# Kernel tuning notes

Measured on AMD Instinct MI355X. Metric: run time of the kernel, lower is better.

Reference implementation:

```python
import jax, jax.numpy as jnp
import numpy as np

EPS = 1e-8  # torch F.cosine_similarity eps


def setup_inputs() -> dict:
    key = jax.random.key(0)
    k1, _ = jax.random.split(key)
    h = jax.random.normal(k1, (8, 2048, 128), dtype=jnp.float32)  # [B, N, D]
    temperature = jnp.array(1.0, dtype=jnp.float32)  # learnable scalar param
    return {"h": h, "temperature": temperature}


def reference(h, temperature):
    # Cosine similarity = (h_i . h_j) / (max(||h_i||, eps) * max(||h_j||, eps)).
    # Normalize rows first, then a single GEMM -> avoids the O(N^2*D) broadcast
    # intermediate the torch code materializes.
    norm = jnp.maximum(jnp.linalg.norm(h, axis=-1, keepdims=True), EPS)  # [B, N, 1]
    hn = h / norm                                                        # [B, N, D]
    sim = jnp.einsum("bnd,bmd->bnm", hn, hn)                             # [B, N, N]
    adj = jax.nn.softmax(sim / temperature, axis=-1)
    return adj
```

## Files before the change

### kernel.cpp

```cpp
#include <hip/hip_runtime.h>
#include <hip/hip_bf16.h>
#include <stdint.h>

#define NB 8
#define NN 2048
#define ND 128

typedef __attribute__((ext_vector_type(8))) short short8;
typedef __attribute__((ext_vector_type(4))) float f32x4;

__device__ __forceinline__ uint32_t pack_bf16(float a, float b) {
    unsigned short ua = __builtin_bit_cast(unsigned short, __float2bfloat16(a));
    unsigned short ub = __builtin_bit_cast(unsigned short, __float2bfloat16(b));
    return (uint32_t)ua | ((uint32_t)ub << 16);
}
__device__ __forceinline__ float unpk_lo(uint32_t p) { return __builtin_bit_cast(float, p << 16); }
__device__ __forceinline__ float unpk_hi(uint32_t p) { return __builtin_bit_cast(float, p & 0xffff0000u); }

__global__ __launch_bounds__(256) void adjnorm_kernel(const float* __restrict__ h,
                                                      unsigned short* __restrict__ hn) {
    const int row  = blockIdx.x * 4 + (threadIdx.x >> 6);
    const int lane = threadIdx.x & 63;
    const float2 v = reinterpret_cast<const float2*>(h + (size_t)row * ND)[lane];
    float ss = v.x * v.x + v.y * v.y;
    #pragma unroll
    for (int m = 32; m >= 1; m >>= 1) ss += __shfl_xor(ss, m);
    const float nrm = fmaxf(sqrtf(ss), 1e-8f);
    const float inv = 1.0f / nrm;
    reinterpret_cast<uint32_t*>(hn + (size_t)row * ND)[lane] = pack_bf16(v.x * inv, v.y * inv);
}

__global__ __launch_bounds__(512) void adjmain_kernel(const unsigned short* __restrict__ hn,
                                                      const float* __restrict__ tptr,
                                                      float* __restrict__ out) {
    const int b       = blockIdx.y;
    const int rowBase = blockIdx.x * 32;
    const int lane = threadIdx.x & 63;
    const int wid  = threadIdx.x >> 6;
    const int cq   = wid & 3;
    const int rh   = wid >> 2;
    const int l15  = lane & 15;
    const int g    = lane >> 4;

    const float invt = 1.0f / tptr[0];

    const unsigned short* Hb = hn + (size_t)b * NN * ND;

    short8 afrag[4];
    {
        const unsigned short* ap = Hb + (size_t)(rowBase + rh * 16 + l15) * ND + g * 8;
        #pragma unroll
        for (int c = 0; c < 4; ++c)
            afrag[c] = *reinterpret_cast<const short8*>(ap + c * 32);
    }

    const int colBase = cq * 512;
    float rs[4] = {0.f, 0.f, 0.f, 0.f};
    uint32_t pp[32][2];

    #pragma unroll
    for (int t = 0; t < 32; ++t) {
        const unsigned short* bp = Hb + (size_t)(colBase + t * 16 + l15) * ND + g * 8;
        f32x4 acc = {0.f, 0.f, 0.f, 0.f};
        #pragma unroll
        for (int c = 0; c < 4; ++c) {
            const short8 bfrag = *reinterpret_cast<const short8*>(bp + c * 32);
            acc = __builtin_amdgcn_mfma_f32_16x16x32_bf16(afrag[c], bfrag, acc, 0, 0, 0);
        }
        const float p0 = __expf((acc[0] - 1.0f) * invt);
        const float p1 = __expf((acc[1] - 1.0f) * invt);
        const float p2 = __expf((acc[2] - 1.0f) * invt);
        const float p3 = __expf((acc[3] - 1.0f) * invt);
        rs[0] += p0; rs[1] += p1; rs[2] += p2; rs[3] += p3;
        pp[t][0] = pack_bf16(p0, p1);
        pp[t][1] = pack_bf16(p2, p3);
    }

    #pragma unroll
    for (int r = 0; r < 4; ++r) {
        #pragma unroll
        for (int m = 1; m < 16; m <<= 1) rs[r] += __shfl_xor(rs[r], m);
    }

    __shared__ float rsum_lds[2][4][16];
    if (l15 == 0) {
        #pragma unroll
        for (int r = 0; r < 4; ++r) rsum_lds[rh][cq][g * 4 + r] = rs[r];
    }
    __syncthreads();
    float invs[4];
    #pragma unroll
    for (int r = 0; r < 4; ++r) {
        const int rr = g * 4 + r;
        const float s = rsum_lds[rh][0][rr] + rsum_lds[rh][1][rr] +
                        rsum_lds[rh][2][rr] + rsum_lds[rh][3][rr];
        invs[r] = 1.0f / s;
    }

    float* orow = out + ((size_t)b * NN + rowBase + rh * 16 + g * 4) * NN + colBase + l15;
    #pragma unroll
    for (int t = 0; t < 32; ++t) {
        const int co = t * 16;
        orow[(size_t)0 * NN + co] = unpk_lo(pp[t][0]) * invs[0];
        orow[(size_t)1 * NN + co] = unpk_hi(pp[t][0]) * invs[1];
        orow[(size_t)2 * NN + co] = unpk_lo(pp[t][1]) * invs[2];
        orow[(size_t)3 * NN + co] = unpk_hi(pp[t][1]) * invs[3];
    }
}

extern "C" void kernel_launch(void* const* d_in, const int* in_sizes, int n_in,
                              void* d_out, int out_size, void* d_ws, size_t ws_size,
                              hipStream_t stream) {
    const float* h  = (const float*)d_in[0];
    const float* tp = (const float*)d_in[1];
    unsigned short* hn = (unsigned short*)d_ws;
    float* out = (float*)d_out;

    hipLaunchKernelGGL(adjnorm_kernel, dim3(NB * NN / 4), dim3(256), 0, stream, h, hn);
    hipLaunchKernelGGL(adjmain_kernel, dim3(NN / 32, NB), dim3(512), 0, stream, hn, tp, out);
}
```

Baseline: 203.0 us.

## Use 16-row blocks with 8 column-split waves and double-buffer B loads

```diff
diff --git a/kernel.cpp b/kernel.cpp
--- a/kernel.cpp
+++ b/kernel.cpp
@@ -34,11 +34,9 @@
                                                       const float* __restrict__ tptr,
                                                       float* __restrict__ out) {
     const int b       = blockIdx.y;
-    const int rowBase = blockIdx.x * 32;
+    const int rowBase = blockIdx.x * 16;
     const int lane = threadIdx.x & 63;
-    const int wid  = threadIdx.x >> 6;
-    const int cq   = wid & 3;
-    const int rh   = wid >> 2;
+    const int w    = threadIdx.x >> 6;
     const int l15  = lane & 15;
     const int g    = lane >> 4;
 
@@ -48,33 +46,51 @@
 
     short8 afrag[4];
     {
-        const unsigned short* ap = Hb + (size_t)(rowBase + rh * 16 + l15) * ND + g * 8;
+        const unsigned short* ap = Hb + (size_t)(rowBase + l15) * ND + g * 8;
         #pragma unroll
         for (int c = 0; c < 4; ++c)
             afrag[c] = *reinterpret_cast<const short8*>(ap + c * 32);
     }
 
-    const int colBase = cq * 512;
+    const unsigned short* colPtr = Hb + (size_t)(w * 256 + l15) * ND + g * 8;
+
     float rs[4] = {0.f, 0.f, 0.f, 0.f};
-    uint32_t pp[32][2];
+    uint32_t pp[16][2];
+    short8 bA[4], bB[4];
 
+#define LOADB(dst, T) do {                                                      \
+        const unsigned short* _bp = colPtr + (size_t)(T) * 16 * ND;             \
+        dst[0] = *reinterpret_cast<const short8*>(_bp);                         \
+        dst[1] = *reinterpret_cast<const short8*>(_bp + 32);                    \
+        dst[2] = *reinterpret_cast<const short8*>(_bp + 64);                    \
+        dst[3] = *reinterpret_cast<const short8*>(_bp + 96);                    \
+    } while (0)
+
+#define COMPUTE(T, BUF) do {                                                    \
+        f32x4 acc = {0.f, 0.f, 0.f, 0.f};                                       \
+        acc = __builtin_amdgcn_mfma_f32_16x16x32_bf16(afrag[0], BUF[0], acc, 0, 0, 0); \
+        acc = __builtin_amdgcn_mfma_f32_16x16x32_bf16(afrag[1], BUF[1], acc, 0, 0, 0); \
+        acc = __builtin_amdgcn_mfma_f32_16x16x32_bf16(afrag[2], BUF[2], acc, 0, 0, 0); \
+        acc = __builtin_amdgcn_mfma_f32_16x16x32_bf16(afrag[3], BUF[3], acc, 0, 0, 0); \
+        const float p0 = __expf((acc[0] - 1.0f) * invt);                        \
+        const float p1 = __expf((acc[1] - 1.0f) * invt);                        \
+        const float p2 = __expf((acc[2] - 1.0f) * invt);                        \
+        const float p3 = __expf((acc[3] - 1.0f) * invt);                        \
+        rs[0] += p0; rs[1] += p1; rs[2] += p2; rs[3] += p3;                     \
+        pp[T][0] = pack_bf16(p0, p1);                                           \
+        pp[T][1] = pack_bf16(p2, p3);                                           \
+    } while (0)
+
+    LOADB(bA, 0);
     #pragma unroll
-    for (int t = 0; t < 32; ++t) {
-        const unsigned short* bp = Hb + (size_t)(colBase + t * 16 + l15) * ND + g * 8;
-        f32x4 acc = {0.f, 0.f, 0.f, 0.f};
-        #pragma unroll
-        for (int c = 0; c < 4; ++c) {
-            const short8 bfrag = *reinterpret_cast<const short8*>(bp + c * 32);
-            acc = __builtin_amdgcn_mfma_f32_16x16x32_bf16(afrag[c], bfrag, acc, 0, 0, 0);
-        }
-        const float p0 = __expf((acc[0] - 1.0f) * invt);
-        const float p1 = __expf((acc[1] - 1.0f) * invt);
-        const float p2 = __expf((acc[2] - 1.0f) * invt);
-        const float p3 = __expf((acc[3] - 1.0f) * invt);
-        rs[0] += p0; rs[1] += p1; rs[2] += p2; rs[3] += p3;
-        pp[t][0] = pack_bf16(p0, p1);
-        pp[t][1] = pack_bf16(p2, p3);
+    for (int tt = 0; tt < 8; ++tt) {
+        LOADB(bB, 2 * tt + 1);
+        COMPUTE(2 * tt, bA);
+        if (tt < 7) LOADB(bA, 2 * tt + 2);
+        COMPUTE(2 * tt + 1, bB);
     }
+#undef LOADB
+#undef COMPUTE
 
     #pragma unroll
     for (int r = 0; r < 4; ++r) {
@@ -82,24 +98,25 @@
         for (int m = 1; m < 16; m <<= 1) rs[r] += __shfl_xor(rs[r], m);
     }
 
-    __shared__ float rsum_lds[2][4][16];
+    __shared__ float rsum_lds[8][16];
     if (l15 == 0) {
         #pragma unroll
-        for (int r = 0; r < 4; ++r) rsum_lds[rh][cq][g * 4 + r] = rs[r];
+        for (int r = 0; r < 4; ++r) rsum_lds[w][g * 4 + r] = rs[r];
     }
     __syncthreads();
     float invs[4];
     #pragma unroll
     for (int r = 0; r < 4; ++r) {
         const int rr = g * 4 + r;
-        const float s = rsum_lds[rh][0][rr] + rsum_lds[rh][1][rr] +
-                        rsum_lds[rh][2][rr] + rsum_lds[rh][3][rr];
+        float s = 0.f;
+        #pragma unroll
+        for (int ww = 0; ww < 8; ++ww) s += rsum_lds[ww][rr];
         invs[r] = 1.0f / s;
     }
 
-    float* orow = out + ((size_t)b * NN + rowBase + rh * 16 + g * 4) * NN + colBase + l15;
+    float* orow = out + ((size_t)b * NN + rowBase + g * 4) * NN + w * 256 + l15;
     #pragma unroll
-    for (int t = 0; t < 32; ++t) {
+    for (int t = 0; t < 16; ++t) {
         const int co = t * 16;
         orow[(size_t)0 * NN + co] = unpk_lo(pp[t][0]) * invs[0];
         orow[(size_t)1 * NN + co] = unpk_hi(pp[t][0]) * invs[1];
@@ -117,5 +134,5 @@
     float* out = (float*)d_out;
 
     hipLaunchKernelGGL(adjnorm_kernel, dim3(NB * NN / 4), dim3(256), 0, stream, h, hn);
-    hipLaunchKernelGGL(adjmain_kernel, dim3(NN / 32, NB), dim3(512), 0, stream, hn, tp, out);
+    hipLaunchKernelGGL(adjmain_kernel, dim3(NN / 16, NB), dim3(512), 0, stream, hn, tp, out);
 }
```

Measured after the change: 197.9 us. 2.5% less time.

## Stage B tiles in LDS via async global_load_lds and transpose MFMA for vector stores

Applied to the files above, without the earlier changes.

```diff
diff --git a/kernel.cpp b/kernel.cpp
--- a/kernel.cpp
+++ b/kernel.cpp
@@ -5,6 +5,7 @@
 #define NB 8
 #define NN 2048
 #define ND 128
+#define NT 32
 
 typedef __attribute__((ext_vector_type(8))) short short8;
 typedef __attribute__((ext_vector_type(4))) float f32x4;
@@ -16,6 +17,12 @@
 }
 __device__ __forceinline__ float unpk_lo(uint32_t p) { return __builtin_bit_cast(float, p << 16); }
 __device__ __forceinline__ float unpk_hi(uint32_t p) { return __builtin_bit_cast(float, p & 0xffff0000u); }
+
+__device__ __forceinline__ void gload_lds16(const void* g, void* l) {
+    __builtin_amdgcn_global_load_lds(
+        (const __attribute__((address_space(1))) unsigned int*)g,
+        (__attribute__((address_space(3))) unsigned int*)l, 16, 0, 0);
+}
 
 __global__ __launch_bounds__(256) void adjnorm_kernel(const float* __restrict__ h,
                                                       unsigned short* __restrict__ hn) {
@@ -30,9 +37,9 @@
     reinterpret_cast<uint32_t*>(hn + (size_t)row * ND)[lane] = pack_bf16(v.x * inv, v.y * inv);
 }
 
-__global__ __launch_bounds__(512) void adjmain_kernel(const unsigned short* __restrict__ hn,
-                                                      const float* __restrict__ tptr,
-                                                      float* __restrict__ out) {
+__global__ __launch_bounds__(512, 4) void adjmain_kernel(const unsigned short* __restrict__ hn,
+                                                         const float* __restrict__ tptr,
+                                                         float* __restrict__ out) {
     const int b       = blockIdx.y;
     const int rowBase = blockIdx.x * 32;
     const int lane = threadIdx.x & 63;
@@ -43,8 +50,10 @@
     const int g    = lane >> 4;
 
     const float invt = 1.0f / tptr[0];
+    const unsigned short* Hb = hn + (size_t)b * NN * ND;
 
-    const unsigned short* Hb = hn + (size_t)b * NN * ND;
+    __shared__ char btile[2][4][4096];
+    __shared__ float rsum_lds[2][4][16];
 
     short8 afrag[4];
     {
@@ -54,57 +63,71 @@
             afrag[c] = *reinterpret_cast<const short8*>(ap + c * 32);
     }
 
-    const int colBase = cq * 512;
-    float rs[4] = {0.f, 0.f, 0.f, 0.f};
-    uint32_t pp[32][2];
+    const unsigned short* gsrc[4];
+    if (rh == 0) {
+        #pragma unroll
+        for (int i = 0; i < 4; ++i) {
+            const int P = i * 1024 + lane * 16;
+            const int L = P ^ (((P >> 8) & 7) << 4);
+            gsrc[i] = Hb + (size_t)(cq * 512 + (L >> 8)) * ND + ((L & 255) >> 1);
+        }
+    }
 
+#define STAGE(T, D) do {                                                \
+        char* _lb = &btile[D][cq][0];                                   \
+        const size_t _o = (size_t)(T) * 16 * ND;                        \
+        gload_lds16(gsrc[0] + _o, _lb);                                 \
+        gload_lds16(gsrc[1] + _o, _lb + 1024);                          \
+        gload_lds16(gsrc[2] + _o, _lb + 2048);                          \
+        gload_lds16(gsrc[3] + _o, _lb + 3072);                          \
+    } while (0)
+
+    int rdo[4];
     #pragma unroll
-    for (int t = 0; t < 32; ++t) {
-        const unsigned short* bp = Hb + (size_t)(colBase + t * 16 + l15) * ND + g * 8;
+    for (int c = 0; c < 4; ++c) {
+        const int Lr = l15 * 256 + g * 16 + c * 64;
+        rdo[c] = Lr ^ ((l15 & 7) << 4);
+    }
+
+    if (rh == 0) STAGE(0, 0);
+    __syncthreads();
+
+    float rs = 0.f;
+    uint32_t pp[NT][2];
+    #pragma unroll
+    for (int t = 0; t < NT; ++t) {
+        if (rh == 0 && t + 1 < NT) STAGE(t + 1, (t + 1) & 1);
+        const char* tb = &btile[t & 1][cq][0];
         f32x4 acc = {0.f, 0.f, 0.f, 0.f};
         #pragma unroll
         for (int c = 0; c < 4; ++c) {
-            const short8 bfrag = *reinterpret_cast<const short8*>(bp + c * 32);
-            acc = __builtin_amdgcn_mfma_f32_16x16x32_bf16(afrag[c], bfrag, acc, 0, 0, 0);
+            const short8 bf = *reinterpret_cast<const short8*>(tb + rdo[c]);
+            acc = __builtin_amdgcn_mfma_f32_16x16x32_bf16(bf, afrag[c], acc, 0, 0, 0);
         }
         const float p0 = __expf((acc[0] - 1.0f) * invt);
         const float p1 = __expf((acc[1] - 1.0f) * invt);
         const float p2 = __expf((acc[2] - 1.0f) * invt);
         const float p3 = __expf((acc[3] - 1.0f) * invt);
-        rs[0] += p0; rs[1] += p1; rs[2] += p2; rs[3] += p3;
+        rs += (p0 + p1) + (p2 + p3);
         pp[t][0] = pack_bf16(p0, p1);
         pp[t][1] = pack_bf16(p2, p3);
+        __syncthreads();
     }
+#undef STAGE
 
+    rs += __shfl_xor(rs, 16);
+    rs += __shfl_xor(rs, 32);
+    if (g == 0) rsum_lds[rh][cq][l15] = rs;
+    __syncthreads();
+    const float inv = 1.0f / (rsum_lds[rh][0][l15] + rsum_lds[rh][1][l15] +
+                              rsum_lds[rh][2][l15] + rsum_lds[rh][3][l15]);
+
+    float* orow = out + ((size_t)b * NN + rowBase + rh * 16 + l15) * NN + cq * 512 + g * 4;
     #pragma unroll
-    for (int r = 0; r < 4; ++r) {
-        #pragma unroll
-        for (int m = 1; m < 16; m <<= 1) rs[r] += __shfl_xor(rs[r], m);
-    }
-
-    __shared__ float rsum_lds[2][4][16];
-    if (l15 == 0) {
-        #pragma unroll
-        for (int r = 0; r < 4; ++r) rsum_lds[rh][cq][g * 4 + r] = rs[r];
-    }
-    __syncthreads();
-    float invs[4];
-    #pragma unroll
-    for (int r = 0; r < 4; ++r) {
-        const int rr = g * 4 + r;
-        const float s = rsum_lds[rh][0][rr] + rsum_lds[rh][1][rr] +
-                        rsum_lds[rh][2][rr] + rsum_lds[rh][3][rr];
-        invs[r] = 1.0f / s;
-    }
-
-    float* orow = out + ((size_t)b * NN + rowBase + rh * 16 + g * 4) * NN + colBase + l15;
-    #pragma unroll
-    for (int t = 0; t < 32; ++t) {
-        const int co = t * 16;
-        orow[(size_t)0 * NN + co] = unpk_lo(pp[t][0]) * invs[0];
-        orow[(size_t)1 * NN + co] = unpk_hi(pp[t][0]) * invs[1];
-        orow[(size_t)2 * NN + co] = unpk_lo(pp[t][1]) * invs[2];
-        orow[(size_t)3 * NN + co] = unpk_hi(pp[t][1]) * invs[3];
+    for (int t = 0; t < NT; ++t) {
+        float4 v = make_float4(unpk_lo(pp[t][0]) * inv, unpk_hi(pp[t][0]) * inv,
+                               unpk_lo(pp[t][1]) * inv, unpk_hi(pp[t][1]) * inv);
+        *reinterpret_cast<float4*>(orow + t * 16) = v;
     }
 }
 
```

Result: slower. 214.5 us (+5.6%).

## Split softmax into rowsum pass and recompute pass with vectorized stores

Applied to the files above, without the earlier changes.

```diff
diff --git a/kernel.cpp b/kernel.cpp
--- a/kernel.cpp
+++ b/kernel.cpp
@@ -14,8 +14,6 @@
     unsigned short ub = __builtin_bit_cast(unsigned short, __float2bfloat16(b));
     return (uint32_t)ua | ((uint32_t)ub << 16);
 }
-__device__ __forceinline__ float unpk_lo(uint32_t p) { return __builtin_bit_cast(float, p << 16); }
-__device__ __forceinline__ float unpk_hi(uint32_t p) { return __builtin_bit_cast(float, p & 0xffff0000u); }
 
 __global__ __launch_bounds__(256) void adjnorm_kernel(const float* __restrict__ h,
                                                       unsigned short* __restrict__ hn) {
@@ -30,81 +28,100 @@
     reinterpret_cast<uint32_t*>(hn + (size_t)row * ND)[lane] = pack_bf16(v.x * inv, v.y * inv);
 }
 
-__global__ __launch_bounds__(512) void adjmain_kernel(const unsigned short* __restrict__ hn,
-                                                      const float* __restrict__ tptr,
-                                                      float* __restrict__ out) {
+
+__global__ __launch_bounds__(256, 4) void rowsum_kernel(const unsigned short* __restrict__ hn,
+                                                        const float* __restrict__ tptr,
+                                                        float* __restrict__ invsum) {
     const int b       = blockIdx.y;
-    const int rowBase = blockIdx.x * 32;
+    const int rowBase = blockIdx.x * 16;
     const int lane = threadIdx.x & 63;
-    const int wid  = threadIdx.x >> 6;
-    const int cq   = wid & 3;
-    const int rh   = wid >> 2;
+    const int w    = threadIdx.x >> 6;
     const int l15  = lane & 15;
     const int g    = lane >> 4;
 
     const float invt = 1.0f / tptr[0];
-
     const unsigned short* Hb = hn + (size_t)b * NN * ND;
 
     short8 afrag[4];
     {
-        const unsigned short* ap = Hb + (size_t)(rowBase + rh * 16 + l15) * ND + g * 8;
+        const unsigned short* ap = Hb + (size_t)(rowBase + l15) * ND + g * 8;
         #pragma unroll
         for (int c = 0; c < 4; ++c)
             afrag[c] = *reinterpret_cast<const short8*>(ap + c * 32);
     }
+    const unsigned short* colPtr = Hb + (size_t)(w * 512 + l15) * ND + g * 8;
 
-    const int colBase = cq * 512;
-    float rs[4] = {0.f, 0.f, 0.f, 0.f};
-    uint32_t pp[32][2];
+    float rsum = 0.f;
+    #pragma unroll 8
+    for (int t = 0; t < 32; ++t) {
+        const unsigned short* bp = colPtr + (size_t)t * 16 * ND;
+        short8 bf0 = *reinterpret_cast<const short8*>(bp);
+        short8 bf1 = *reinterpret_cast<const short8*>(bp + 32);
+        short8 bf2 = *reinterpret_cast<const short8*>(bp + 64);
+        short8 bf3 = *reinterpret_cast<const short8*>(bp + 96);
+        f32x4 acc = {0.f, 0.f, 0.f, 0.f};
+        acc = __builtin_amdgcn_mfma_f32_16x16x32_bf16(bf0, afrag[0], acc, 0, 0, 0);
+        acc = __builtin_amdgcn_mfma_f32_16x16x32_bf16(bf1, afrag[1], acc, 0, 0, 0);
+        acc = __builtin_amdgcn_mfma_f32_16x16x32_bf16(bf2, afrag[2], acc, 0, 0, 0);
+        acc = __builtin_amdgcn_mfma_f32_16x16x32_bf16(bf3, afrag[3], acc, 0, 0, 0);
+        rsum += __expf((acc[0] - 1.0f) * invt) + __expf((acc[1] - 1.0f) * invt)
+              + __expf((acc[2] - 1.0f) * invt) + __expf((acc[3] - 1.0f) * invt);
+    }
+    rsum += __shfl_xor(rsum, 16);
+    rsum += __shfl_xor(rsum, 32);
 
-    #pragma unroll
+    __shared__ float sm[4][16];
+    if (lane < 16) sm[w][l15] = rsum;
+    __syncthreads();
+    if (threadIdx.x < 16) {
+        const float s = sm[0][threadIdx.x] + sm[1][threadIdx.x] +
+                        sm[2][threadIdx.x] + sm[3][threadIdx.x];
+        invsum[(size_t)b * NN + rowBase + threadIdx.x] = 1.0f / s;
+    }
+}
+
+__global__ __launch_bounds__(256, 4) void adjmain_kernel(const unsigned short* __restrict__ hn,
+                                                         const float* __restrict__ tptr,
+                                                         const float* __restrict__ invsum,
+                                                         float* __restrict__ out) {
+    const int b       = blockIdx.y;
+    const int rowBase = blockIdx.x * 16;
+    const int lane = threadIdx.x & 63;
+    const int w    = threadIdx.x >> 6;
+    const int l15  = lane & 15;
+    const int g    = lane >> 4;
+
+    const float invt = 1.0f / tptr[0];
+    const unsigned short* Hb = hn + (size_t)b * NN * ND;
+    const float invs = invsum[(size_t)b * NN + rowBase + l15];
+
+    short8 afrag[4];
+    {
+        const unsigned short* ap = Hb + (size_t)(rowBase + l15) * ND + g * 8;
+        #pragma unroll
+        for (int c = 0; c < 4; ++c)
+            afrag[c] = *reinterpret_cast<const short8*>(ap + c * 32);
+    }
+    const unsigned short* colPtr = Hb + (size_t)(w * 512 + l15) * ND + g * 8;
+    float* orow = out + ((size_t)b * NN + rowBase + l15) * NN + w * 512 + g * 4;
+
+    #pragma unroll 8
     for (int t = 0; t < 32; ++t) {
-        const unsigned short* bp = Hb + (size_t)(colBase + t * 16 + l15) * ND + g * 8;
+        const unsigned short* bp = colPtr + (size_t)t * 16 * ND;
+        short8 bf0 = *reinterpret_cast<const short8*>(bp);
+        short8 bf1 = *reinterpret_cast<const short8*>(bp + 32);
+        short8 bf2 = *reinterpret_cast<const short8*>(bp + 64);
+        short8 bf3 = *reinterpret_cast<const short8*>(bp + 96);
         f32x4 acc = {0.f, 0.f, 0.f, 0.f};
-        #pragma unroll
-        for (int c = 0; c < 4; ++c) {
-            const short8 bfrag = *reinterpret_cast<const short8*>(bp + c * 32);
-            acc = __builtin_amdgcn_mfma_f32_16x16x32_bf16(afrag[c], bfrag, acc, 0, 0, 0);
-        }
-        const float p0 = __expf((acc[0] - 1.0f) * invt);
-        const float p1 = __expf((acc[1] - 1.0f) * invt);
-        const float p2 = __expf((acc[2] - 1.0f) * invt);
-        const float p3 = __expf((acc[3] - 1.0f) * invt);
-        rs[0] += p0; rs[1] += p1; rs[2] += p2; rs[3] += p3;
-        pp[t][0] = pack_bf16(p0, p1);
-        pp[t][1] = pack_bf16(p2, p3);
-    }
-
-    #pragma unroll
-    for (int r = 0; r < 4; ++r) {
-        #pragma unroll
-        for (int m = 1; m < 16; m <<= 1) rs[r] += __shfl_xor(rs[r], m);
-    }
-
-    __shared__ float rsum_lds[2][4][16];
-    if (l15 == 0) {
-        #pragma unroll
-        for (int r = 0; r < 4; ++r) rsum_lds[rh][cq][g * 4 + r] = rs[r];
-    }
-    __syncthreads();
-    float invs[4];
-    #pragma unroll
-    for (int r = 0; r < 4; ++r) {
-        const int rr = g * 4 + r;
-        const float s = rsum_lds[rh][0][rr] + rsum_lds[rh][1][rr] +
-                        rsum_lds[rh][2][rr] + rsum_lds[rh][3][rr];
-        invs[r] = 1.0f / s;
-    }
-
-    float* orow = out + ((size_t)b * NN + rowBase + rh * 16 + g * 4) * NN + colBase + l15;
-    #pragma unroll
-    for (int t = 0; t < 32; ++t) {
-        const int co = t * 16;
-        orow[(size_t)0 * NN + co] = unpk_lo(pp[t][0]) * invs[0];
-        orow[(size_t)1 * NN + co] = unpk_hi(pp[t][0]) * invs[1];
-        orow[(size_t)2 * NN + co] = unpk_lo(pp[t][1]) * invs[2];
-        orow[(size_t)3 * NN + co] = unpk_hi(pp[t][1]) * invs[3];
+        acc = __builtin_amdgcn_mfma_f32_16x16x32_bf16(bf0, afrag[0], acc, 0, 0, 0);
+        acc = __builtin_amdgcn_mfma_f32_16x16x32_bf16(bf1, afrag[1], acc, 0, 0, 0);
+        acc = __builtin_amdgcn_mfma_f32_16x16x32_bf16(bf2, afrag[2], acc, 0, 0, 0);
+        acc = __builtin_amdgcn_mfma_f32_16x16x32_bf16(bf3, afrag[3], acc, 0, 0, 0);
+        const float4 v = make_float4(__expf((acc[0] - 1.0f) * invt) * invs,
+                                     __expf((acc[1] - 1.0f) * invt) * invs,
+                                     __expf((acc[2] - 1.0f) * invt) * invs,
+                                     __expf((acc[3] - 1.0f) * invt) * invs);
+        *reinterpret_cast<float4*>(orow + t * 16) = v;
     }
 }
 
@@ -114,8 +131,10 @@
     const float* h  = (const float*)d_in[0];
     const float* tp = (const float*)d_in[1];
     unsigned short* hn = (unsigned short*)d_ws;
+    float* invsum = (float*)((char*)d_ws + (size_t)NB * NN * ND * 2);
     float* out = (float*)d_out;
 
     hipLaunchKernelGGL(adjnorm_kernel, dim3(NB * NN / 4), dim3(256), 0, stream, h, hn);
-    hipLaunchKernelGGL(adjmain_kernel, dim3(NN / 32, NB), dim3(512), 0, stream, hn, tp, out);
+    hipLaunchKernelGGL(rowsum_kernel,  dim3(NN / 16, NB), dim3(256), 0, stream, hn, tp, invsum);
+    hipLaunchKernelGGL(adjmain_kernel, dim3(NN / 16, NB), dim3(256), 0, stream, hn, tp, invsum, out);
 }
```

Result: slower. 244.7 us (+20.5%).
